# Optimization experiments

Hardware: AMD Instinct MI355X
Metric: run time of the kernel (lower is better)

Reference implementation:

```python
import jax, jax.numpy as jnp
import numpy as np

N_NODES = 50000
N_EDGES = 1600000
DIM = 128
EDGE_DIM = 16
IN_DIM = 2 * DIM + EDGE_DIM


def setup_inputs() -> dict:
    key = jax.random.key(0)
    ks = jax.random.split(key, 8)
    h = jax.random.normal(ks[0], (N_NODES, DIM), dtype=jnp.float32)
    src = jax.random.randint(ks[1], (N_EDGES,), 0, N_NODES)
    dst = jax.random.randint(ks[2], (N_EDGES,), 0, N_NODES)
    edge_attr = jax.random.normal(ks[3], (N_EDGES, EDGE_DIM), dtype=jnp.float32)
    # Linear weights stored as [in, out] so x @ W + b
    W1 = jax.random.normal(ks[4], (IN_DIM, DIM), dtype=jnp.float32) / np.sqrt(IN_DIM)
    b1 = jnp.zeros((DIM,), dtype=jnp.float32)
    W2 = jax.random.normal(ks[5], (DIM, DIM), dtype=jnp.float32) / np.sqrt(DIM)
    b2 = jnp.zeros((DIM,), dtype=jnp.float32)
    gamma = jnp.ones((DIM,), dtype=jnp.float32)
    beta = jnp.zeros((DIM,), dtype=jnp.float32)
    return {"h": h, "src": src, "dst": dst, "edge_attr": edge_attr,
            "W1": W1, "b1": b1, "W2": W2, "b2": b2, "gamma": gamma, "beta": beta}


def _layer_norm(x, gamma, beta, eps=1e-5):
    mu = jnp.mean(x, axis=-1, keepdims=True)
    var = jnp.mean(jnp.square(x - mu), axis=-1, keepdims=True)
    return (x - mu) * jax.lax.rsqrt(var + eps) * gamma + beta


def reference(h, src, dst, edge_attr, W1, b1, W2, b2, gamma, beta):
    # gather endpoint features + edge attrs -> [E, 2*dim+edge_dim]
    x = jnp.concatenate([h[src], h[dst], edge_attr], axis=-1)
    hdn = jax.nn.gelu(x @ W1 + b1, approximate=False)  # torch nn.GELU default is exact
    messages = hdn @ W2 + b2                           # [E, dim]
    # scatter-add messages to destination nodes
    agg = jax.ops.segment_sum(messages, dst, num_segments=h.shape[0])
    return _layer_norm(h + agg, gamma, beta)
```

## Files before the change

kernel.cpp:

```cpp
#include <hip/hip_runtime.h>
#include <math.h>

#define NUM_NODES 50000
#define NUM_EDGES 1600000
#define DIM 128
#define EDGE_DIM 16
#define NKT1 18
#define NKT2 8
#define MT 64
#define XSTRIDE 296
#define CSTRIDE 132
#define NSCAN 196

typedef short bf16x8 __attribute__((ext_vector_type(8)));
typedef float floatx16 __attribute__((ext_vector_type(16)));
typedef unsigned short ushort4v __attribute__((ext_vector_type(4)));
typedef unsigned short ushort8v __attribute__((ext_vector_type(8)));

__device__ __forceinline__ unsigned short f2b(float f) {
    unsigned u = __builtin_bit_cast(unsigned, f);
    u += 0x7FFFu + ((u >> 16) & 1u);
    return (unsigned short)(u >> 16);
}

__global__ void prep_kernel(const float* __restrict__ W1, const float* __restrict__ W2,
                            short* __restrict__ W1f, short* __restrict__ W2f)
{
    int gid = blockIdx.x * 256 + threadIdx.x;
    if (gid < NKT1 * 4 * 64) {
        int lane = gid & 63, nb = (gid >> 6) & 3, kt = gid >> 8;
        int n = nb * 32 + (lane & 31);
        int kbase = kt * 16 + (lane >> 5) * 8;
        #pragma unroll
        for (int j = 0; j < 8; ++j) {
            int k = kbase + j;
            W1f[gid * 8 + j] = (k < 272) ? (short)f2b(W1[(size_t)k * DIM + n]) : (short)0;
        }
    } else if (gid < NKT1 * 4 * 64 + NKT2 * 4 * 64) {
        int g2 = gid - NKT1 * 4 * 64;
        int lane = g2 & 63, nb = (g2 >> 6) & 3, kt = g2 >> 8;
        int n = nb * 32 + (lane & 31);
        int kbase = kt * 16 + (lane >> 5) * 8;
        #pragma unroll
        for (int j = 0; j < 8; ++j)
            W2f[g2 * 8 + j] = (short)f2b(W2[(size_t)(kbase + j) * DIM + n]);
    }
}

__global__ void hconv_kernel(const float* __restrict__ h, unsigned short* __restrict__ h_bf) {
    int t = blockIdx.x * 256 + threadIdx.x;
    float4 v = ((const float4*)h)[t];
    ushort4v o;
    o.x = f2b(v.x); o.y = f2b(v.y); o.z = f2b(v.z); o.w = f2b(v.w);
    ((ushort4v*)h_bf)[t] = o;
}

__global__ void hist_kernel(const int* __restrict__ dst, int* __restrict__ counts) {
    int e = blockIdx.x * 256 + threadIdx.x;
    atomicAdd(&counts[dst[e]], 1);
}

__global__ void scanA_kernel(const int* __restrict__ counts, int* __restrict__ bsum) {
    __shared__ int sb[256];
    int t = threadIdx.x, i = blockIdx.x * 256 + t;
    int v = (i < NUM_NODES) ? counts[i] : 0;
    sb[t] = v; __syncthreads();
    for (int off = 1; off < 256; off <<= 1) {
        int x = (t >= off) ? sb[t - off] : 0;
        __syncthreads(); sb[t] += x; __syncthreads();
    }
    if (t == 255) bsum[blockIdx.x] = sb[255];
}

__global__ void scanB_kernel(const int* __restrict__ bsum, int* __restrict__ boffs) {
    __shared__ int sb[256];
    int t = threadIdx.x;
    int v = (t < NSCAN) ? bsum[t] : 0;
    sb[t] = v; __syncthreads();
    for (int off = 1; off < 256; off <<= 1) {
        int x = (t >= off) ? sb[t - off] : 0;
        __syncthreads(); sb[t] += x; __syncthreads();
    }
    if (t < NSCAN) boffs[t] = sb[t] - v;
}

__global__ void scanC_kernel(const int* __restrict__ counts, const int* __restrict__ boffs,
                             int* __restrict__ cursor) {
    __shared__ int sb[256];
    int t = threadIdx.x, i = blockIdx.x * 256 + t;
    int v = (i < NUM_NODES) ? counts[i] : 0;
    sb[t] = v; __syncthreads();
    for (int off = 1; off < 256; off <<= 1) {
        int x = (t >= off) ? sb[t - off] : 0;
        __syncthreads(); sb[t] += x; __syncthreads();
    }
    if (i < NUM_NODES) cursor[i] = boffs[blockIdx.x] + sb[t] - v;
}

__global__ void scatter2_kernel(const int* __restrict__ src, const int* __restrict__ dst,
                                const float* __restrict__ ea, int* __restrict__ cursor,
                                int* __restrict__ src_s, int* __restrict__ dst_s,
                                unsigned short* __restrict__ ea_s)
{
    int e = blockIdx.x * 256 + threadIdx.x;
    int d = dst[e];
    int p = atomicAdd(&cursor[d], 1);
    src_s[p] = src[e];
    dst_s[p] = d;
    const float4* er = (const float4*)(ea + (size_t)e * EDGE_DIM);
    __attribute__((aligned(16))) unsigned short tmp[16];
    #pragma unroll
    for (int c = 0; c < 4; ++c) {
        float4 v = er[c];
        tmp[c * 4 + 0] = f2b(v.x); tmp[c * 4 + 1] = f2b(v.y);
        tmp[c * 4 + 2] = f2b(v.z); tmp[c * 4 + 3] = f2b(v.w);
    }
    ushort8v* o = (ushort8v*)(ea_s + (size_t)p * EDGE_DIM);
    o[0] = *(ushort8v*)&tmp[0];
    o[1] = *(ushort8v*)&tmp[8];
}

__global__ __launch_bounds__(256, 4) void edge_sorted_kernel(
    const unsigned short* __restrict__ h_bf,
    const int* __restrict__ src_s, const int* __restrict__ dst_s,
    const unsigned short* __restrict__ ea_s,
    const short* __restrict__ W1f, const short* __restrict__ W2f,
    const float* __restrict__ pb1, const float* __restrict__ pb2,
    float* __restrict__ agg)
{
    __shared__ __align__(16) short xbuf[MT * XSTRIDE];
    __shared__ int srcl[MT];
    __shared__ int dstl[MT];
    short* hdnf = xbuf;
    float* cbuf = (float*)xbuf;

    const int tid = threadIdx.x;
    const long long base = (long long)blockIdx.x * MT;

    if (tid < MT)            srcl[tid]      = src_s[base + tid];
    else if (tid < 2 * MT)   dstl[tid - MT] = dst_s[base + tid - MT];
    __syncthreads();

    #pragma unroll
    for (int it = 0; it < 8; ++it) {
        int g = it * 256 + tid;
        int row = g >> 5, c = g & 31;
        const ushort8v* p = (c < 16)
            ? (const ushort8v*)(h_bf + (size_t)srcl[row] * DIM + c * 8)
            : (const ushort8v*)(h_bf + (size_t)dstl[row] * DIM + (c - 16) * 8);
        *(ushort8v*)&xbuf[row * XSTRIDE + c * 8] = *p;
    }
    if (tid < 128) {
        int row = tid >> 1, c = tid & 1;
        *(ushort8v*)&xbuf[row * XSTRIDE + 256 + c * 8] =
            *(const ushort8v*)(ea_s + (size_t)(base + row) * EDGE_DIM + c * 8);
    } else {
        int t2 = tid - 128;
        int row = t2 >> 1, c = t2 & 1;
        ushort8v z = {0, 0, 0, 0, 0, 0, 0, 0};
        *(ushort8v*)&xbuf[row * XSTRIDE + 272 + c * 8] = z;
    }
    __syncthreads();

    const int lane = tid & 63, wave = tid >> 6;
    const int rm = wave >> 1, rn = wave & 1;
    const int lm = lane & 31, half = lane >> 5;

    floatx16 acc0 = {}, acc1 = {};
    #pragma unroll
    for (int kt = 0; kt < NKT1; ++kt) {
        bf16x8 a  = *(const bf16x8*)&xbuf[(rm * 32 + lm) * XSTRIDE + kt * 16 + half * 8];
        bf16x8 b0 = *(const bf16x8*)(W1f + ((kt * 4 + rn * 2 + 0) * 64 + lane) * 8);
        bf16x8 b1 = *(const bf16x8*)(W1f + ((kt * 4 + rn * 2 + 1) * 64 + lane) * 8);
        acc0 = __builtin_amdgcn_mfma_f32_32x32x16_bf16(a, b0, acc0, 0, 0, 0);
        acc1 = __builtin_amdgcn_mfma_f32_32x32x16_bf16(a, b1, acc1, 0, 0, 0);
    }
    __syncthreads();

    #pragma unroll
    for (int j = 0; j < 2; ++j) {
        int kg = rn * 64 + j * 32 + lm;
        float bb = pb1[kg];
        int ktl = kg >> 4, lrb = 32 * ((kg >> 3) & 1), jr = kg & 7;
        const floatx16& A = j ? acc1 : acc0;
        #pragma unroll
        for (int r = 0; r < 16; ++r) {
            int rr = (r & 3) + 8 * (r >> 2) + 4 * half;
            float v = A[r] + bb;
            float u = v * (1.5957691216f + 0.0713548163f * v * v);
            u = fminf(u, 80.f);
            float t = __expf(u);
            float g = v * t * __builtin_amdgcn_rcpf(t + 1.f);
            hdnf[((rm * 8 + ktl) * 64 + rr + lrb) * 8 + jr] = (short)f2b(g);
        }
    }
    __syncthreads();

    floatx16 acc2_0 = {}, acc2_1 = {};
    #pragma unroll
    for (int kt = 0; kt < NKT2; ++kt) {
        bf16x8 a  = *(const bf16x8*)&hdnf[((rm * 8 + kt) * 64 + lane) * 8];
        bf16x8 b0 = *(const bf16x8*)(W2f + ((kt * 4 + rn * 2 + 0) * 64 + lane) * 8);
        bf16x8 b1 = *(const bf16x8*)(W2f + ((kt * 4 + rn * 2 + 1) * 64 + lane) * 8);
        acc2_0 = __builtin_amdgcn_mfma_f32_32x32x16_bf16(a, b0, acc2_0, 0, 0, 0);
        acc2_1 = __builtin_amdgcn_mfma_f32_32x32x16_bf16(a, b1, acc2_1, 0, 0, 0);
    }
    __syncthreads();

    #pragma unroll
    for (int j = 0; j < 2; ++j) {
        int col = rn * 64 + j * 32 + lm;
        float bb = pb2[col];
        const floatx16& A = j ? acc2_1 : acc2_0;
        #pragma unroll
        for (int r = 0; r < 16; ++r) {
            int rr = (r & 3) + 8 * (r >> 2) + 4 * half;
            cbuf[(rm * 32 + rr) * CSTRIDE + col] = A[r] + bb;
        }
    }
    __syncthreads();

    {
        int col = tid & 127, hf = tid >> 7;
        int r0 = hf * 32, r1 = r0 + 32;
        float s = 0.f;
        int cur = dstl[r0];
        for (int r = r0; r < r1; ++r) {
            s += cbuf[r * CSTRIDE + col];
            int nxt = (r == r1 - 1) ? -1 : dstl[r + 1];
            if (nxt != cur) {
                atomicAdd(&agg[(size_t)cur * DIM + col], s);
                s = 0.f;
                cur = nxt;
            }
        }
    }
}

__global__ __launch_bounds__(256, 2) void edge_atomic_kernel(
    const float* __restrict__ h, const int* __restrict__ src, const int* __restrict__ dst,
    const float* __restrict__ ea, const short* __restrict__ W1f, const short* __restrict__ W2f,
    const float* __restrict__ pb1, const float* __restrict__ pb2, float* __restrict__ agg)
{
    __shared__ __align__(16) short xbuf[128 * 296];
    __shared__ int srcl[128];
    __shared__ int dstl[128];
    short* hdnf = xbuf;

    const int tid = threadIdx.x;
    const long long base = (long long)blockIdx.x * 128;
    if (tid < 128) srcl[tid] = src[base + tid];
    else           dstl[tid - 128] = dst[base + (tid - 128)];
    __syncthreads();
    for (int it = 0; it < 37; ++it) {
        int i = tid + it * 256;
        int row = i / 74, c = i - row * 74;
        float4 v = make_float4(0.f, 0.f, 0.f, 0.f);
        if (c < 32)      v = *(const float4*)(h + (size_t)srcl[row] * DIM + c * 4);
        else if (c < 64) v = *(const float4*)(h + (size_t)dstl[row] * DIM + (c - 32) * 4);
        else if (c < 68) v = *(const float4*)(ea + (size_t)(base + row) * EDGE_DIM + (c - 64) * 4);
        ushort4v o;
        o.x = f2b(v.x); o.y = f2b(v.y); o.z = f2b(v.z); o.w = f2b(v.w);
        *(ushort4v*)&xbuf[row * 296 + c * 4] = o;
    }
    __syncthreads();
    const int lane = tid & 63, wave = tid >> 6;
    const int rm = wave >> 1, rn = wave & 1;
    const int lm = lane & 31, half = lane >> 5;
    floatx16 acc[2][2] = {};
    #pragma unroll
    for (int kt = 0; kt < NKT1; ++kt) {
        bf16x8 a0 = *(const bf16x8*)&xbuf[(rm * 64 + lm) * 296 + kt * 16 + half * 8];
        bf16x8 a1 = *(const bf16x8*)&xbuf[(rm * 64 + 32 + lm) * 296 + kt * 16 + half * 8];
        bf16x8 b0 = *(const bf16x8*)(W1f + ((kt * 4 + rn * 2 + 0) * 64 + lane) * 8);
        bf16x8 b1 = *(const bf16x8*)(W1f + ((kt * 4 + rn * 2 + 1) * 64 + lane) * 8);
        acc[0][0] = __builtin_amdgcn_mfma_f32_32x32x16_bf16(a0, b0, acc[0][0], 0, 0, 0);
        acc[0][1] = __builtin_amdgcn_mfma_f32_32x32x16_bf16(a0, b1, acc[0][1], 0, 0, 0);
        acc[1][0] = __builtin_amdgcn_mfma_f32_32x32x16_bf16(a1, b0, acc[1][0], 0, 0, 0);
        acc[1][1] = __builtin_amdgcn_mfma_f32_32x32x16_bf16(a1, b1, acc[1][1], 0, 0, 0);
    }
    __syncthreads();
    float bb1_0 = pb1[rn * 64 + lm];
    float bb1_1 = pb1[rn * 64 + 32 + lm];
    #pragma unroll
    for (int i = 0; i < 2; ++i)
        #pragma unroll
        for (int j = 0; j < 2; ++j) {
            float bb = j ? bb1_1 : bb1_0;
            int kg = rn * 64 + j * 32 + lm;
            int ktl = kg >> 4;
            int lrbase = 32 * ((lm >> 3) & 1);
            int jr = lm & 7;
            #pragma unroll
            for (int r = 0; r < 16; ++r) {
                int rr = (r & 3) + 8 * (r >> 2) + 4 * half;
                float v = acc[i][j][r] + bb;
                float u = v * (1.5957691216f + 0.0713548163f * v * v);
                u = fminf(u, 80.f);
                float t = __expf(u);
                float g = v * t * __builtin_amdgcn_rcpf(t + 1.f);
                hdnf[(((rm * 2 + i) * 8 + ktl) * 64 + rr + lrbase) * 8 + jr] = (short)f2b(g);
            }
        }
    __syncthreads();
    floatx16 acc2[2][2] = {};
    #pragma unroll
    for (int kt = 0; kt < NKT2; ++kt) {
        bf16x8 a0 = *(const bf16x8*)&hdnf[(((rm * 2 + 0) * 8 + kt) * 64 + lane) * 8];
        bf16x8 a1 = *(const bf16x8*)&hdnf[(((rm * 2 + 1) * 8 + kt) * 64 + lane) * 8];
        bf16x8 b0 = *(const bf16x8*)(W2f + ((kt * 4 + rn * 2 + 0) * 64 + lane) * 8);
        bf16x8 b1 = *(const bf16x8*)(W2f + ((kt * 4 + rn * 2 + 1) * 64 + lane) * 8);
        acc2[0][0] = __builtin_amdgcn_mfma_f32_32x32x16_bf16(a0, b0, acc2[0][0], 0, 0, 0);
        acc2[0][1] = __builtin_amdgcn_mfma_f32_32x32x16_bf16(a0, b1, acc2[0][1], 0, 0, 0);
        acc2[1][0] = __builtin_amdgcn_mfma_f32_32x32x16_bf16(a1, b0, acc2[1][0], 0, 0, 0);
        acc2[1][1] = __builtin_amdgcn_mfma_f32_32x32x16_bf16(a1, b1, acc2[1][1], 0, 0, 0);
    }
    float bb2_0 = pb2[rn * 64 + lm];
    float bb2_1 = pb2[rn * 64 + 32 + lm];
    #pragma unroll
    for (int i = 0; i < 2; ++i)
        #pragma unroll
        for (int j = 0; j < 2; ++j) {
            float bb = j ? bb2_1 : bb2_0;
            int n = rn * 64 + j * 32 + lm;
            #pragma unroll
            for (int r = 0; r < 16; ++r) {
                int rr = (r & 3) + 8 * (r >> 2) + 4 * half;
                atomicAdd(&agg[(size_t)dstl[rm * 64 + i * 32 + rr] * DIM + n],
                          acc2[i][j][r] + bb);
            }
        }
}

__global__ __launch_bounds__(256) void ln_kernel(
    const float* __restrict__ h, float* __restrict__ io,
    const float* __restrict__ gamma, const float* __restrict__ beta)
{
    int wave = threadIdx.x >> 6, lane = threadIdx.x & 63;
    int node = blockIdx.x * 4 + wave;
    const float2* h2 = (const float2*)(h + (size_t)node * DIM);
    float2* o2 = (float2*)(io + (size_t)node * DIM);
    float2 a = o2[lane];
    float2 b = h2[lane];
    float x0 = a.x + b.x, x1 = a.y + b.y;
    float s = x0 + x1;
    float ss = x0 * x0 + x1 * x1;
    #pragma unroll
    for (int m = 1; m < 64; m <<= 1) {
        s  += __shfl_xor(s, m, 64);
        ss += __shfl_xor(ss, m, 64);
    }
    float mu = s * (1.f / DIM);
    float var = ss * (1.f / DIM) - mu * mu;
    float rs = rsqrtf(var + 1e-5f);
    float g0 = gamma[lane * 2], g1 = gamma[lane * 2 + 1];
    float e0 = beta[lane * 2],  e1 = beta[lane * 2 + 1];
    float2 outv;
    outv.x = (x0 - mu) * rs * g0 + e0;
    outv.y = (x1 - mu) * rs * g1 + e1;
    o2[lane] = outv;
}

extern "C" void kernel_launch(void* const* d_in, const int* in_sizes, int n_in,
                              void* d_out, int out_size, void* d_ws, size_t ws_size,
                              hipStream_t stream)
{
    const float* h     = (const float*)d_in[0];
    const int*   src   = (const int*)d_in[1];
    const int*   dst   = (const int*)d_in[2];
    const float* ea    = (const float*)d_in[3];
    const float* W1    = (const float*)d_in[4];
    const float* pb1   = (const float*)d_in[5];
    const float* W2    = (const float*)d_in[6];
    const float* pb2   = (const float*)d_in[7];
    const float* gamma = (const float*)d_in[8];
    const float* beta  = (const float*)d_in[9];
    float* out = (float*)d_out;

    char* ws = (char*)d_ws;
    short* W1f   = (short*)ws;
    short* W2f   = (short*)(ws + 73728);
    int* counts  = (int*)(ws + 106496);
    int* cursor  = (int*)(ws + 306496);
    int* bsum    = (int*)(ws + 506496);
    int* boffs   = (int*)(ws + 507520);
    int* src_s   = (int*)(ws + 508544);
    int* dst_s   = (int*)(ws + 6908544);
    unsigned short* h_bf = (unsigned short*)(ws + 13308544);
    unsigned short* ea_s = (unsigned short*)(ws + 26108544);
    const size_t REQUIRED = 77308544;

    hipMemsetAsync(d_out, 0, (size_t)NUM_NODES * DIM * sizeof(float), stream);
    prep_kernel<<<26, 256, 0, stream>>>(W1, W2, W1f, W2f);

    if (ws_size >= REQUIRED) {
        hipMemsetAsync(counts, 0, NUM_NODES * sizeof(int), stream);
        hconv_kernel<<<6250, 256, 0, stream>>>(h, h_bf);
        hist_kernel<<<NUM_EDGES / 256, 256, 0, stream>>>(dst, counts);
        scanA_kernel<<<NSCAN, 256, 0, stream>>>(counts, bsum);
        scanB_kernel<<<1, 256, 0, stream>>>(bsum, boffs);
        scanC_kernel<<<NSCAN, 256, 0, stream>>>(counts, boffs, cursor);
        scatter2_kernel<<<NUM_EDGES / 256, 256, 0, stream>>>(src, dst, ea, cursor,
                                                             src_s, dst_s, ea_s);
        edge_sorted_kernel<<<NUM_EDGES / MT, 256, 0, stream>>>(
            h_bf, src_s, dst_s, ea_s, W1f, W2f, pb1, pb2, out);
    } else {
        edge_atomic_kernel<<<NUM_EDGES / 128, 256, 0, stream>>>(
            h, src, dst, ea, W1f, W2f, pb1, pb2, out);
    }
    ln_kernel<<<NUM_NODES / 4, 256, 0, stream>>>(h, out, gamma, beta);
}
```

Before: 678.6 us.

## Move second linear layer after scatter-add using linearity; fuse node GEMM with LayerNorm

Because the second linear layer is linear, the per-edge GELU outputs are now scatter-summed per destination node first. W2 is then applied once per node, with the bias scaled by the node's in-degree. This cuts the second GEMM from one per edge to one per node. A new node kernel does that GEMM, adds h and applies LayerNorm in one pass. Edge attributes are gathered through a permutation index instead of being pre-sorted. The change also drops the fallback atomic path and the workspace size check, and it rounds the aggregated sums to bf16 before the W2 GEMM.

Result: faster. 619.0 us (-8.8%).

```diff
diff --git a/kernel.cpp b/kernel.cpp
--- a/kernel.cpp
+++ b/kernel.cpp
@@ -8,9 +8,9 @@
 #define NKT1 18
 #define NKT2 8
 #define MT 64
-#define XSTRIDE 296
 #define CSTRIDE 132
 #define NSCAN 196
+#define NODE_BLOCKS ((NUM_NODES + 63) / 64)
 
 typedef short bf16x8 __attribute__((ext_vector_type(8)));
 typedef float floatx16 __attribute__((ext_vector_type(16)));
@@ -97,92 +97,79 @@
     if (i < NUM_NODES) cursor[i] = boffs[blockIdx.x] + sb[t] - v;
 }
 
-__global__ void scatter2_kernel(const int* __restrict__ src, const int* __restrict__ dst,
-                                const float* __restrict__ ea, int* __restrict__ cursor,
-                                int* __restrict__ src_s, int* __restrict__ dst_s,
-                                unsigned short* __restrict__ ea_s)
+__global__ void scatter3_kernel(const int* __restrict__ src, const int* __restrict__ dst,
+                                int* __restrict__ cursor, int* __restrict__ src_s,
+                                int* __restrict__ dst_s, int* __restrict__ eid_s)
 {
     int e = blockIdx.x * 256 + threadIdx.x;
     int d = dst[e];
     int p = atomicAdd(&cursor[d], 1);
     src_s[p] = src[e];
     dst_s[p] = d;
-    const float4* er = (const float4*)(ea + (size_t)e * EDGE_DIM);
-    __attribute__((aligned(16))) unsigned short tmp[16];
-    #pragma unroll
-    for (int c = 0; c < 4; ++c) {
-        float4 v = er[c];
-        tmp[c * 4 + 0] = f2b(v.x); tmp[c * 4 + 1] = f2b(v.y);
-        tmp[c * 4 + 2] = f2b(v.z); tmp[c * 4 + 3] = f2b(v.w);
-    }
-    ushort8v* o = (ushort8v*)(ea_s + (size_t)p * EDGE_DIM);
-    o[0] = *(ushort8v*)&tmp[0];
-    o[1] = *(ushort8v*)&tmp[8];
-}
-
-__global__ __launch_bounds__(256, 4) void edge_sorted_kernel(
+    eid_s[p] = e;
+}
+
+__global__ __launch_bounds__(256, 4) void edge_kernel(
     const unsigned short* __restrict__ h_bf,
     const int* __restrict__ src_s, const int* __restrict__ dst_s,
-    const unsigned short* __restrict__ ea_s,
-    const short* __restrict__ W1f, const short* __restrict__ W2f,
-    const float* __restrict__ pb1, const float* __restrict__ pb2,
-    float* __restrict__ agg)
-{
-    __shared__ __align__(16) short xbuf[MT * XSTRIDE];
-    __shared__ int srcl[MT];
-    __shared__ int dstl[MT];
-    short* hdnf = xbuf;
+    const int* __restrict__ eid_s, const float* __restrict__ ea,
+    const short* __restrict__ W1f, const float* __restrict__ pb1,
+    float* __restrict__ aggh)
+{
+    __shared__ __align__(16) short xbuf[36 * 64 * 8];
+    __shared__ int srcl[MT], dstl[MT], eidl[MT];
     float* cbuf = (float*)xbuf;
 
     const int tid = threadIdx.x;
     const long long base = (long long)blockIdx.x * MT;
 
-    if (tid < MT)            srcl[tid]      = src_s[base + tid];
-    else if (tid < 2 * MT)   dstl[tid - MT] = dst_s[base + tid - MT];
+    if (tid < MT)            srcl[tid]          = src_s[base + tid];
+    else if (tid < 2 * MT)   dstl[tid - MT]     = dst_s[base + tid - MT];
+    else if (tid < 3 * MT)   eidl[tid - 2 * MT] = eid_s[base + tid - 2 * MT];
     __syncthreads();
 
     #pragma unroll
     for (int it = 0; it < 8; ++it) {
         int g = it * 256 + tid;
-        int row = g >> 5, c = g & 31;
-        const ushort8v* p = (c < 16)
-            ? (const ushort8v*)(h_bf + (size_t)srcl[row] * DIM + c * 8)
-            : (const ushort8v*)(h_bf + (size_t)dstl[row] * DIM + (c - 16) * 8);
-        *(ushort8v*)&xbuf[row * XSTRIDE + c * 8] = *p;
-    }
-    if (tid < 128) {
-        int row = tid >> 1, c = tid & 1;
-        *(ushort8v*)&xbuf[row * XSTRIDE + 256 + c * 8] =
-            *(const ushort8v*)(ea_s + (size_t)(base + row) * EDGE_DIM + c * 8);
-    } else {
-        int t2 = tid - 128;
-        int row = t2 >> 1, c = t2 & 1;
-        ushort8v z = {0, 0, 0, 0, 0, 0, 0, 0};
-        *(ushort8v*)&xbuf[row * XSTRIDE + 272 + c * 8] = z;
+        int kt2 = g >> 6, row = g & 63;
+        int node = (kt2 < 16) ? srcl[row] : dstl[row];
+        ushort8v v = *(const ushort8v*)(h_bf + (size_t)node * DIM + (kt2 & 15) * 8);
+        *(ushort8v*)&xbuf[(kt2 * 64 + row) * 8] = v;
+    }
+    {
+        int row = (tid & 127) >> 1, hc = tid & 1;
+        if (tid < 128) {
+            const float4* er = (const float4*)(ea + (size_t)eidl[row] * EDGE_DIM + hc * 8);
+            float4 v0 = er[0], v1 = er[1];
+            ushort8v o;
+            o[0] = f2b(v0.x); o[1] = f2b(v0.y); o[2] = f2b(v0.z); o[3] = f2b(v0.w);
+            o[4] = f2b(v1.x); o[5] = f2b(v1.y); o[6] = f2b(v1.z); o[7] = f2b(v1.w);
+            *(ushort8v*)&xbuf[((32 + hc) * 64 + row) * 8] = o;
+        } else {
+            ushort8v z = {0, 0, 0, 0, 0, 0, 0, 0};
+            *(ushort8v*)&xbuf[((34 + hc) * 64 + row) * 8] = z;
+        }
     }
     __syncthreads();
 
     const int lane = tid & 63, wave = tid >> 6;
-    const int rm = wave >> 1, rn = wave & 1;
     const int lm = lane & 31, half = lane >> 5;
 
     floatx16 acc0 = {}, acc1 = {};
     #pragma unroll
     for (int kt = 0; kt < NKT1; ++kt) {
-        bf16x8 a  = *(const bf16x8*)&xbuf[(rm * 32 + lm) * XSTRIDE + kt * 16 + half * 8];
-        bf16x8 b0 = *(const bf16x8*)(W1f + ((kt * 4 + rn * 2 + 0) * 64 + lane) * 8);
-        bf16x8 b1 = *(const bf16x8*)(W1f + ((kt * 4 + rn * 2 + 1) * 64 + lane) * 8);
-        acc0 = __builtin_amdgcn_mfma_f32_32x32x16_bf16(a, b0, acc0, 0, 0, 0);
-        acc1 = __builtin_amdgcn_mfma_f32_32x32x16_bf16(a, b1, acc1, 0, 0, 0);
-    }
-    __syncthreads();
-
-    #pragma unroll
-    for (int j = 0; j < 2; ++j) {
-        int kg = rn * 64 + j * 32 + lm;
-        float bb = pb1[kg];
-        int ktl = kg >> 4, lrb = 32 * ((kg >> 3) & 1), jr = kg & 7;
-        const floatx16& A = j ? acc1 : acc0;
+        bf16x8 a0 = *(const bf16x8*)&xbuf[((kt * 2 + half) * 64 + lm) * 8];
+        bf16x8 a1 = *(const bf16x8*)&xbuf[((kt * 2 + half) * 64 + 32 + lm) * 8];
+        bf16x8 b  = *(const bf16x8*)(W1f + ((kt * 4 + wave) * 64 + lane) * 8);
+        acc0 = __builtin_amdgcn_mfma_f32_32x32x16_bf16(a0, b, acc0, 0, 0, 0);
+        acc1 = __builtin_amdgcn_mfma_f32_32x32x16_bf16(a1, b, acc1, 0, 0, 0);
+    }
+    __syncthreads();
+
+    float bb = pb1[wave * 32 + lm];
+    #pragma unroll
+    for (int s = 0; s < 2; ++s) {
+        const floatx16& A = s ? acc1 : acc0;
         #pragma unroll
         for (int r = 0; r < 16; ++r) {
             int rr = (r & 3) + 8 * (r >> 2) + 4 * half;
@@ -191,31 +178,7 @@
             u = fminf(u, 80.f);
             float t = __expf(u);
             float g = v * t * __builtin_amdgcn_rcpf(t + 1.f);
-            hdnf[((rm * 8 + ktl) * 64 + rr + lrb) * 8 + jr] = (short)f2b(g);
-        }
-    }
-    __syncthreads();
-
-    floatx16 acc2_0 = {}, acc2_1 = {};
-    #pragma unroll
-    for (int kt = 0; kt < NKT2; ++kt) {
-        bf16x8 a  = *(const bf16x8*)&hdnf[((rm * 8 + kt) * 64 + lane) * 8];
-        bf16x8 b0 = *(const bf16x8*)(W2f + ((kt * 4 + rn * 2 + 0) * 64 + lane) * 8);
-        bf16x8 b1 = *(const bf16x8*)(W2f + ((kt * 4 + rn * 2 + 1) * 64 + lane) * 8);
-        acc2_0 = __builtin_amdgcn_mfma_f32_32x32x16_bf16(a, b0, acc2_0, 0, 0, 0);
-        acc2_1 = __builtin_amdgcn_mfma_f32_32x32x16_bf16(a, b1, acc2_1, 0, 0, 0);
-    }
-    __syncthreads();
-
-    #pragma unroll
-    for (int j = 0; j < 2; ++j) {
-        int col = rn * 64 + j * 32 + lm;
-        float bb = pb2[col];
-        const floatx16& A = j ? acc2_1 : acc2_0;
-        #pragma unroll
-        for (int r = 0; r < 16; ++r) {
-            int rr = (r & 3) + 8 * (r >> 2) + 4 * half;
-            cbuf[(rm * 32 + rr) * CSTRIDE + col] = A[r] + bb;
+            cbuf[(s * 32 + rr) * CSTRIDE + wave * 32 + lm] = g;
         }
     }
     __syncthreads();
@@ -229,7 +192,7 @@
             s += cbuf[r * CSTRIDE + col];
             int nxt = (r == r1 - 1) ? -1 : dstl[r + 1];
             if (nxt != cur) {
-                atomicAdd(&agg[(size_t)cur * DIM + col], s);
+                atomicAdd(&aggh[(size_t)cur * DIM + col], s);
                 s = 0.f;
                 cur = nxt;
             }
@@ -237,128 +200,102 @@
     }
 }
 
-__global__ __launch_bounds__(256, 2) void edge_atomic_kernel(
-    const float* __restrict__ h, const int* __restrict__ src, const int* __restrict__ dst,
-    const float* __restrict__ ea, const short* __restrict__ W1f, const short* __restrict__ W2f,
-    const float* __restrict__ pb1, const float* __restrict__ pb2, float* __restrict__ agg)
-{
-    __shared__ __align__(16) short xbuf[128 * 296];
-    __shared__ int srcl[128];
-    __shared__ int dstl[128];
-    short* hdnf = xbuf;
+__global__ __launch_bounds__(256, 4) void node_ln_kernel(
+    const float* __restrict__ aggh, const int* __restrict__ counts,
+    const short* __restrict__ W2f, const float* __restrict__ pb2,
+    const float* __restrict__ h, const float* __restrict__ gamma,
+    const float* __restrict__ beta, float* __restrict__ out)
+{
+    __shared__ __align__(16) float sbuf[64 * CSTRIDE];
+    __shared__ int cntl[64];
+    short* abuf = (short*)sbuf;
 
     const int tid = threadIdx.x;
-    const long long base = (long long)blockIdx.x * 128;
-    if (tid < 128) srcl[tid] = src[base + tid];
-    else           dstl[tid - 128] = dst[base + (tid - 128)];
-    __syncthreads();
-    for (int it = 0; it < 37; ++it) {
-        int i = tid + it * 256;
-        int row = i / 74, c = i - row * 74;
-        float4 v = make_float4(0.f, 0.f, 0.f, 0.f);
-        if (c < 32)      v = *(const float4*)(h + (size_t)srcl[row] * DIM + c * 4);
-        else if (c < 64) v = *(const float4*)(h + (size_t)dstl[row] * DIM + (c - 32) * 4);
-        else if (c < 68) v = *(const float4*)(ea + (size_t)(base + row) * EDGE_DIM + (c - 64) * 4);
-        ushort4v o;
-        o.x = f2b(v.x); o.y = f2b(v.y); o.z = f2b(v.z); o.w = f2b(v.w);
-        *(ushort4v*)&xbuf[row * 296 + c * 4] = o;
-    }
-    __syncthreads();
+    const int n0 = blockIdx.x * 64;
+
+    if (tid < 64) {
+        int node = n0 + tid;
+        cntl[tid] = (node < NUM_NODES) ? counts[node] : 0;
+    }
+    #pragma unroll
+    for (int it = 0; it < 4; ++it) {
+        int g = it * 256 + tid;
+        int kt2 = g >> 6, row = g & 63;
+        int node = n0 + row;
+        ushort8v o = {0, 0, 0, 0, 0, 0, 0, 0};
+        if (node < NUM_NODES) {
+            const float4* p = (const float4*)(aggh + (size_t)node * DIM + kt2 * 8);
+            float4 v0 = p[0], v1 = p[1];
+            o[0] = f2b(v0.x); o[1] = f2b(v0.y); o[2] = f2b(v0.z); o[3] = f2b(v0.w);
+            o[4] = f2b(v1.x); o[5] = f2b(v1.y); o[6] = f2b(v1.z); o[7] = f2b(v1.w);
+        }
+        *(ushort8v*)&abuf[(kt2 * 64 + row) * 8] = o;
+    }
+    __syncthreads();
+
     const int lane = tid & 63, wave = tid >> 6;
-    const int rm = wave >> 1, rn = wave & 1;
     const int lm = lane & 31, half = lane >> 5;
-    floatx16 acc[2][2] = {};
-    #pragma unroll
-    for (int kt = 0; kt < NKT1; ++kt) {
-        bf16x8 a0 = *(const bf16x8*)&xbuf[(rm * 64 + lm) * 296 + kt * 16 + half * 8];
-        bf16x8 a1 = *(const bf16x8*)&xbuf[(rm * 64 + 32 + lm) * 296 + kt * 16 + half * 8];
-        bf16x8 b0 = *(const bf16x8*)(W1f + ((kt * 4 + rn * 2 + 0) * 64 + lane) * 8);
-        bf16x8 b1 = *(const bf16x8*)(W1f + ((kt * 4 + rn * 2 + 1) * 64 + lane) * 8);
-        acc[0][0] = __builtin_amdgcn_mfma_f32_32x32x16_bf16(a0, b0, acc[0][0], 0, 0, 0);
-        acc[0][1] = __builtin_amdgcn_mfma_f32_32x32x16_bf16(a0, b1, acc[0][1], 0, 0, 0);
-        acc[1][0] = __builtin_amdgcn_mfma_f32_32x32x16_bf16(a1, b0, acc[1][0], 0, 0, 0);
-        acc[1][1] = __builtin_amdgcn_mfma_f32_32x32x16_bf16(a1, b1, acc[1][1], 0, 0, 0);
-    }
-    __syncthreads();
-    float bb1_0 = pb1[rn * 64 + lm];
-    float bb1_1 = pb1[rn * 64 + 32 + lm];
-    #pragma unroll
-    for (int i = 0; i < 2; ++i)
+
+    floatx16 acc0 = {}, acc1 = {};
+    #pragma unroll
+    for (int kt = 0; kt < NKT2; ++kt) {
+        bf16x8 a0 = *(const bf16x8*)&abuf[((kt * 2 + half) * 64 + lm) * 8];
+        bf16x8 a1 = *(const bf16x8*)&abuf[((kt * 2 + half) * 64 + 32 + lm) * 8];
+        bf16x8 b  = *(const bf16x8*)(W2f + ((kt * 4 + wave) * 64 + lane) * 8);
+        acc0 = __builtin_amdgcn_mfma_f32_32x32x16_bf16(a0, b, acc0, 0, 0, 0);
+        acc1 = __builtin_amdgcn_mfma_f32_32x32x16_bf16(a1, b, acc1, 0, 0, 0);
+    }
+    __syncthreads();
+
+    float bb2 = pb2[wave * 32 + lm];
+    #pragma unroll
+    for (int s = 0; s < 2; ++s) {
+        const floatx16& A = s ? acc1 : acc0;
         #pragma unroll
-        for (int j = 0; j < 2; ++j) {
-            float bb = j ? bb1_1 : bb1_0;
-            int kg = rn * 64 + j * 32 + lm;
-            int ktl = kg >> 4;
-            int lrbase = 32 * ((lm >> 3) & 1);
-            int jr = lm & 7;
+        for (int r = 0; r < 16; ++r) {
+            int rr = (r & 3) + 8 * (r >> 2) + 4 * half;
+            int row = s * 32 + rr;
+            sbuf[row * CSTRIDE + wave * 32 + lm] = A[r] + (float)cntl[row] * bb2;
+        }
+    }
+    __syncthreads();
+
+    {
+        int row = tid >> 2, q = tid & 3;
+        int node = n0 + row;
+        if (node < NUM_NODES) {
+            float4 xv[8];
+            float s = 0.f, ss = 0.f;
+            const float4* hp = (const float4*)(h + (size_t)node * DIM + q * 32);
             #pragma unroll
-            for (int r = 0; r < 16; ++r) {
-                int rr = (r & 3) + 8 * (r >> 2) + 4 * half;
-                float v = acc[i][j][r] + bb;
-                float u = v * (1.5957691216f + 0.0713548163f * v * v);
-                u = fminf(u, 80.f);
-                float t = __expf(u);
-                float g = v * t * __builtin_amdgcn_rcpf(t + 1.f);
-                hdnf[(((rm * 2 + i) * 8 + ktl) * 64 + rr + lrbase) * 8 + jr] = (short)f2b(g);
+            for (int i = 0; i < 8; ++i) {
+                float4 c = *(const float4*)&sbuf[row * CSTRIDE + q * 32 + i * 4];
+                float4 hh = hp[i];
+                float4 x;
+                x.x = c.x + hh.x; x.y = c.y + hh.y; x.z = c.z + hh.z; x.w = c.w + hh.w;
+                xv[i] = x;
+                s  += x.x + x.y + x.z + x.w;
+                ss += x.x * x.x + x.y * x.y + x.z * x.z + x.w * x.w;
             }
-        }
-    __syncthreads();
-    floatx16 acc2[2][2] = {};
-    #pragma unroll
-    for (int kt = 0; kt < NKT2; ++kt) {
-        bf16x8 a0 = *(const bf16x8*)&hdnf[(((rm * 2 + 0) * 8 + kt) * 64 + lane) * 8];
-        bf16x8 a1 = *(const bf16x8*)&hdnf[(((rm * 2 + 1) * 8 + kt) * 64 + lane) * 8];
-        bf16x8 b0 = *(const bf16x8*)(W2f + ((kt * 4 + rn * 2 + 0) * 64 + lane) * 8);
-        bf16x8 b1 = *(const bf16x8*)(W2f + ((kt * 4 + rn * 2 + 1) * 64 + lane) * 8);
-        acc2[0][0] = __builtin_amdgcn_mfma_f32_32x32x16_bf16(a0, b0, acc2[0][0], 0, 0, 0);
-        acc2[0][1] = __builtin_amdgcn_mfma_f32_32x32x16_bf16(a0, b1, acc2[0][1], 0, 0, 0);
-        acc2[1][0] = __builtin_amdgcn_mfma_f32_32x32x16_bf16(a1, b0, acc2[1][0], 0, 0, 0);
-        acc2[1][1] = __builtin_amdgcn_mfma_f32_32x32x16_bf16(a1, b1, acc2[1][1], 0, 0, 0);
-    }
-    float bb2_0 = pb2[rn * 64 + lm];
-    float bb2_1 = pb2[rn * 64 + 32 + lm];
-    #pragma unroll
-    for (int i = 0; i < 2; ++i)
-        #pragma unroll
-        for (int j = 0; j < 2; ++j) {
-            float bb = j ? bb2_1 : bb2_0;
-            int n = rn * 64 + j * 32 + lm;
+            s  += __shfl_xor(s, 1, 64);  s  += __shfl_xor(s, 2, 64);
+            ss += __shfl_xor(ss, 1, 64); ss += __shfl_xor(ss, 2, 64);
+            float mu = s * (1.f / DIM);
+            float var = ss * (1.f / DIM) - mu * mu;
+            float rs = rsqrtf(var + 1e-5f);
+            const float4* gp = (const float4*)(gamma + q * 32);
+            const float4* bp = (const float4*)(beta + q * 32);
+            float4* op = (float4*)(out + (size_t)node * DIM + q * 32);
             #pragma unroll
-            for (int r = 0; r < 16; ++r) {
-                int rr = (r & 3) + 8 * (r >> 2) + 4 * half;
-                atomicAdd(&agg[(size_t)dstl[rm * 64 + i * 32 + rr] * DIM + n],
-                          acc2[i][j][r] + bb);
+            for (int i = 0; i < 8; ++i) {
+                float4 g4 = gp[i], b4 = bp[i], o;
+                o.x = (xv[i].x - mu) * rs * g4.x + b4.x;
+                o.y = (xv[i].y - mu) * rs * g4.y + b4.y;
+                o.z = (xv[i].z - mu) * rs * g4.z + b4.z;
+                o.w = (xv[i].w - mu) * rs * g4.w + b4.w;
+                op[i] = o;
             }
         }
-}
-
-__global__ __launch_bounds__(256) void ln_kernel(
-    const float* __restrict__ h, float* __restrict__ io,
-    const float* __restrict__ gamma, const float* __restrict__ beta)
-{
-    int wave = threadIdx.x >> 6, lane = threadIdx.x & 63;
-    int node = blockIdx.x * 4 + wave;
-    const float2* h2 = (const float2*)(h + (size_t)node * DIM);
-    float2* o2 = (float2*)(io + (size_t)node * DIM);
-    float2 a = o2[lane];
-    float2 b = h2[lane];
-    float x0 = a.x + b.x, x1 = a.y + b.y;
-    float s = x0 + x1;
-    float ss = x0 * x0 + x1 * x1;
-    #pragma unroll
-    for (int m = 1; m < 64; m <<= 1) {
-        s  += __shfl_xor(s, m, 64);
-        ss += __shfl_xor(ss, m, 64);
-    }
-    float mu = s * (1.f / DIM);
-    float var = ss * (1.f / DIM) - mu * mu;
-    float rs = rsqrtf(var + 1e-5f);
-    float g0 = gamma[lane * 2], g1 = gamma[lane * 2 + 1];
-    float e0 = beta[lane * 2],  e1 = beta[lane * 2 + 1];
-    float2 outv;
-    outv.x = (x0 - mu) * rs * g0 + e0;
-    outv.y = (x1 - mu) * rs * g1 + e1;
-    o2[lane] = outv;
+    }
 }
 
 extern "C" void kernel_launch(void* const* d_in, const int* in_sizes, int n_in,
@@ -386,27 +323,23 @@
     int* boffs   = (int*)(ws + 507520);
     int* src_s   = (int*)(ws + 508544);
     int* dst_s   = (int*)(ws + 6908544);
-    unsigned short* h_bf = (unsigned short*)(ws + 13308544);
-    unsigned short* ea_s = (unsigned short*)(ws + 26108544);
-    const size_t REQUIRED = 77308544;
-
-    hipMemsetAsync(d_out, 0, (size_t)NUM_NODES * DIM * sizeof(float), stream);
+    int* eid_s   = (int*)(ws + 13308544);
+    unsigned short* h_bf = (unsigned short*)(ws + 19708544);
+    float* aggh  = (float*)(ws + 32508544);
+
+    hipMemsetAsync(aggh, 0, (size_t)NUM_NODES * DIM * sizeof(float), stream);
+    hipMemsetAsync(counts, 0, NUM_NODES * sizeof(int), stream);
+
     prep_kernel<<<26, 256, 0, stream>>>(W1, W2, W1f, W2f);
-
-    if (ws_size >= REQUIRED) {
-        hipMemsetAsync(counts, 0, NUM_NODES * sizeof(int), stream);
-        hconv_kernel<<<6250, 256, 0, stream>>>(h, h_bf);
-        hist_kernel<<<NUM_EDGES / 256, 256, 0, stream>>>(dst, counts);
-        scanA_kernel<<<NSCAN, 256, 0, stream>>>(counts, bsum);
-        scanB_kernel<<<1, 256, 0, stream>>>(bsum, boffs);
-        scanC_kernel<<<NSCAN, 256, 0, stream>>>(counts, boffs, cursor);
-        scatter2_kernel<<<NUM_EDGES / 256, 256, 0, stream>>>(src, dst, ea, cursor,
-                                                             src_s, dst_s, ea_s);
-        edge_sorted_kernel<<<NUM_EDGES / MT, 256, 0, stream>>>(
-            h_bf, src_s, dst_s, ea_s, W1f, W2f, pb1, pb2, out);
-    } else {
-        edge_atomic_kernel<<<NUM_EDGES / 128, 256, 0, stream>>>(
-            h, src, dst, ea, W1f, W2f, pb1, pb2, out);
-    }
-    ln_kernel<<<NUM_NODES / 4, 256, 0, stream>>>(h, out, gamma, beta);
-}
+    hconv_kernel<<<6250, 256, 0, stream>>>(h, h_bf);
+    hist_kernel<<<NUM_EDGES / 256, 256, 0, stream>>>(dst, counts);
+    scanA_kernel<<<NSCAN, 256, 0, stream>>>(counts, bsum);
+    scanB_kernel<<<1, 256, 0, stream>>>(bsum, boffs);
+    scanC_kernel<<<NSCAN, 256, 0, stream>>>(counts, boffs, cursor);
+    scatter3_kernel<<<NUM_EDGES / 256, 256, 0, stream>>>(src, dst, cursor,
+                                                         src_s, dst_s, eid_s);
+    edge_kernel<<<NUM_EDGES / MT, 256, 0, stream>>>(h_bf, src_s, dst_s, eid_s, ea,
+                                                    W1f, pb1, aggh);
+    node_ln_kernel<<<NODE_BLOCKS, 256, 0, stream>>>(aggh, counts, W2f, pb2,
+                                                    h, gamma, beta, out);
+}
```
